# Optimization experiments

Measured on AMD Instinct MI355X. Metric: run time of the kernel, lower is better.

## Reference

```python
import jax, jax.numpy as jnp
import numpy as np

B, S = 8, 2048
DQ = DK = DV = 64


def setup_inputs() -> dict:
    key = jax.random.key(0)
    ks = jax.random.split(key, 9)
    s = 1.0 / np.sqrt(DK)
    return {
        "query": jax.random.normal(ks[0], (B, S, DQ), dtype=jnp.float32),
        "key": jax.random.normal(ks[1], (B, S, DK), dtype=jnp.float32),
        "value": jax.random.normal(ks[2], (B, S, DV), dtype=jnp.float32),
        "inv_scale_factor": jnp.ones((1,), dtype=jnp.float32),
        "dropout_p": jnp.zeros((1,), dtype=jnp.float32),
        "Wq": (jax.random.uniform(ks[3], (DQ, DK), jnp.float32, -1, 1) * s),
        "bq": (jax.random.uniform(ks[4], (DK,), jnp.float32, -1, 1) * s),
        "Wk": (jax.random.uniform(ks[5], (DK, DK), jnp.float32, -1, 1) * s),
        "bk": (jax.random.uniform(ks[6], (DK,), jnp.float32, -1, 1) * s),
        "Wv": (jax.random.uniform(ks[7], (DV, DV), jnp.float32, -1, 1) * s),
        "bv": (jax.random.uniform(ks[8], (DV,), jnp.float32, -1, 1) * s),
    }


def reference(query, key, value, inv_scale_factor, dropout_p, Wq, bq, Wk, bk, Wv, bv):
    # Linear projections (torch Linear: x @ W^T + b; here W stored as [in,out])
    q = query @ Wq + bq              # [B,S,DK]
    k = key @ Wk + bk                # [B,S,DK]
    v = value @ Wv + bv              # [B,S,DV]
    qk = jnp.einsum("bqd,bkd->bqk", q, k)      # [B,S,S]
    scaled_qk = qk / inv_scale_factor[0]
    softmax_qk = jax.nn.softmax(scaled_qk, axis=-1)
    # dropout (training semantics of F.dropout): keep mask / (1-p)
    p = dropout_p[0]
    keep = jax.random.uniform(jax.random.key(42), softmax_qk.shape) >= p
    dropout_qk = jnp.where(keep, softmax_qk, 0.0) / (1.0 - p)
    return jnp.einsum("bqk,bkd->bqd", dropout_qk, v)  # [B,S,DV]
```

## Files before the change

kernel.cpp:

```cpp
#include <hip/hip_runtime.h>
#include <hip/hip_bf16.h>

#define B_ 8
#define S_ 2048
#define D_ 64

using short8  = __attribute__((ext_vector_type(8))) short;
using bf16x4  = __attribute__((ext_vector_type(4))) short;
using f32x4   = __attribute__((ext_vector_type(4))) float;
using uint4v  = __attribute__((ext_vector_type(4))) unsigned int;

typedef unsigned short ushort_t;

static __device__ inline unsigned short f2bf(float f) {
  __hip_bfloat16 h = __float2bfloat16(f);
  return *reinterpret_cast<unsigned short*>(&h);
}
static __device__ inline unsigned int packbf(float a, float b) {
  return (unsigned int)f2bf(a) | ((unsigned int)f2bf(b) << 16);
}

__global__ __launch_bounds__(256) void proj_all(
    const float* __restrict__ query, const float* __restrict__ key,
    const float* __restrict__ value, const float* __restrict__ inv_scale,
    const float* __restrict__ Wq, const float* __restrict__ bq,
    const float* __restrict__ Wk, const float* __restrict__ bk,
    const float* __restrict__ Wv, const float* __restrict__ bv,
    ushort_t* __restrict__ qp, ushort_t* __restrict__ kp,
    ushort_t* __restrict__ vt) {
  __shared__ ushort_t wt[64 * 80];

  int t     = blockIdx.x >> 8;
  int r_    = blockIdx.x & 255;
  int chunk = (r_ & 7) * 32 + (r_ >> 3);
  const float* X    = (t == 0) ? query : (t == 1) ? key : value;
  const float* W    = (t == 0) ? Wq    : (t == 1) ? Wk  : Wv;
  const float* bias = (t == 0) ? bq    : (t == 1) ? bk  : bv;
  float qscale = (t == 0) ? (1.44269504f / inv_scale[0]) : 1.0f;

  {
    int k  = threadIdx.x >> 2;
    int c0 = (threadIdx.x & 3) * 16;
    const float* wr = W + k * 64 + c0;
    #pragma unroll
    for (int j = 0; j < 16; j += 4) {
      float4 v4 = *reinterpret_cast<const float4*>(wr + j);
      wt[(c0 + j)     * 80 + k] = f2bf(v4.x);
      wt[(c0 + j + 1) * 80 + k] = f2bf(v4.y);
      wt[(c0 + j + 2) * 80 + k] = f2bf(v4.z);
      wt[(c0 + j + 3) * 80 + k] = f2bf(v4.w);
    }
  }
  __syncthreads();

  int wv = threadIdx.x >> 6, l = threadIdx.x & 63;
  int lm = l & 15, lh = l >> 4;
  int r0 = chunk * 64 + wv * 16;

  const float* xrow = X + (size_t)(r0 + lm) * 64 + lh * 8;
  float4 x0 = *reinterpret_cast<const float4*>(xrow);
  float4 x1 = *reinterpret_cast<const float4*>(xrow + 4);
  float4 x2 = *reinterpret_cast<const float4*>(xrow + 32);
  float4 x3 = *reinterpret_cast<const float4*>(xrow + 36);
  short8 xa0, xa1;
  xa0[0] = f2bf(x0.x); xa0[1] = f2bf(x0.y); xa0[2] = f2bf(x0.z); xa0[3] = f2bf(x0.w);
  xa0[4] = f2bf(x1.x); xa0[5] = f2bf(x1.y); xa0[6] = f2bf(x1.z); xa0[7] = f2bf(x1.w);
  xa1[0] = f2bf(x2.x); xa1[1] = f2bf(x2.y); xa1[2] = f2bf(x2.z); xa1[3] = f2bf(x2.w);
  xa1[4] = f2bf(x3.x); xa1[5] = f2bf(x3.y); xa1[6] = f2bf(x3.z); xa1[7] = f2bf(x3.w);

  f32x4 zero = {0.f, 0.f, 0.f, 0.f};

  #pragma unroll
  for (int c = 0; c < 4; ++c) {
    const ushort_t* wb = &wt[(c * 16 + lm) * 80 + lh * 8];
    short8 wf0 = *reinterpret_cast<const short8*>(wb);
    short8 wf1 = *reinterpret_cast<const short8*>(wb + 32);

    if (t < 2) {
      f32x4 acc = __builtin_amdgcn_mfma_f32_16x16x32_bf16(wf0, xa0, zero, 0, 0, 0);
      acc       = __builtin_amdgcn_mfma_f32_16x16x32_bf16(wf1, xa1, acc,  0, 0, 0);
      float4 bb = *reinterpret_cast<const float4*>(bias + c * 16 + 4 * lh);
      bf16x4 s;
      s[0] = f2bf((acc[0] + bb.x) * qscale);
      s[1] = f2bf((acc[1] + bb.y) * qscale);
      s[2] = f2bf((acc[2] + bb.z) * qscale);
      s[3] = f2bf((acc[3] + bb.w) * qscale);
      ushort_t* dst = (t ? kp : qp) + (size_t)(r0 + lm) * 64 + c * 16 + 4 * lh;
      *reinterpret_cast<bf16x4*>(dst) = s;
    } else {
      f32x4 acc = __builtin_amdgcn_mfma_f32_16x16x32_bf16(xa0, wf0, zero, 0, 0, 0);
      acc       = __builtin_amdgcn_mfma_f32_16x16x32_bf16(xa1, wf1, acc,  0, 0, 0);
      float bb = bias[c * 16 + lm];
      bf16x4 s;
      s[0] = f2bf(acc[0] + bb); s[1] = f2bf(acc[1] + bb);
      s[2] = f2bf(acc[2] + bb); s[3] = f2bf(acc[3] + bb);
      int bb_i = r0 >> 11;
      int rb   = r0 & 2047;
      int blk  = rb >> 5;
      int th   = (rb >> 4) & 1;
      ushort_t* dst = vt + (((size_t)(bb_i * (S_ / 32) + blk) * 64
                             + c * 16 + lm) * 32) + lh * 8 + 4 * th;
      *reinterpret_cast<bf16x4*>(dst) = s;
    }
  }
}

#define ITERS2 16

__global__ __launch_bounds__(512, 2) void attn(
    const ushort_t* __restrict__ qp, const ushort_t* __restrict__ kp,
    const ushort_t* __restrict__ vt,
    const float* __restrict__ dropout_p, float* __restrict__ out) {
  __shared__ ushort_t kst[4][2][2048];
  __shared__ ushort_t vst[4][2][2048];
  __shared__ float obuf[8][64][33];
  __shared__ float lbuf[8][32];

  const int tid = threadIdx.x;
  const int w = tid >> 6, l = tid & 63;
  const int lm = l & 15, lh = l >> 4;
  const int qi = w & 1, kvs = w >> 1;
  const int b  = blockIdx.x & 7;
  const int qg = blockIdx.x >> 3;
  const int qb = qg * 64 + qi * 32;

  float dscale = 1.0f / (1.0f - dropout_p[0]);

  const ushort_t* qbase = qp + ((size_t)(b * S_ + qb + lm)) * D_ + lh * 8;
  short8 qa0 = *reinterpret_cast<const short8*>(qbase);
  short8 qa1 = *reinterpret_cast<const short8*>(qbase + 32);
  short8 qb0 = *reinterpret_cast<const short8*>(qbase + 16 * D_);
  short8 qb1 = *reinterpret_cast<const short8*>(qbase + 16 * D_ + 32);

  const ushort_t* ksrc = kp + (size_t)b * S_ * D_ + (size_t)kvs * 512 * D_;
  const ushort_t* vsrc = vt + (size_t)(b * 64 + kvs * 16) * 2048;
  const ushort_t* src  = qi ? vsrc : ksrc;

  int swoff[4];
  #pragma unroll
  for (int j = 0; j < 4; ++j) {
    int lin = j * 1024 + l * 16;
    int sw  = qi ? (((l >> 2) & 3) << 4) : (((l >> 3) & 7) << 4);
    swoff[j] = lin ^ sw;
  }
  char* dst0 = qi ? (char*)&vst[kvs][0][0] : (char*)&kst[kvs][0][0];

  const char* kstb = (const char*)&kst[kvs][0][0];
  const char* vstb = (const char*)&vst[kvs][0][0];
  const int kro0 = (lm * 128 + lh * 16)        ^ ((lm & 7) << 4);
  const int kro1 = (lm * 128 + 64 + lh * 16)   ^ ((lm & 7) << 4);
  const int kro2 = ((16 + lm) * 128 + lh * 16) ^ ((lm & 7) << 4);
  const int kro3 = ((16 + lm) * 128 + 64 + lh * 16) ^ ((lm & 7) << 4);
  int vro[4];
  #pragma unroll
  for (int dt = 0; dt < 4; ++dt)
    vro[dt] = ((dt * 16 + lm) * 64 + lh * 16) ^ ((lm & 3) << 4);

  {
    short8 s0 = *reinterpret_cast<const short8*>(src + l * 8);
    short8 s1 = *reinterpret_cast<const short8*>(src + 512 + l * 8);
    short8 s2 = *reinterpret_cast<const short8*>(src + 1024 + l * 8);
    short8 s3 = *reinterpret_cast<const short8*>(src + 1536 + l * 8);
    *reinterpret_cast<short8*>(dst0 + swoff[0]) = s0;
    *reinterpret_cast<short8*>(dst0 + swoff[1]) = s1;
    *reinterpret_cast<short8*>(dst0 + swoff[2]) = s2;
    *reinterpret_cast<short8*>(dst0 + swoff[3]) = s3;
  }
  __syncthreads();

  f32x4 zero = {0.f, 0.f, 0.f, 0.f};
  f32x4 oA[4] = {zero, zero, zero, zero};
  f32x4 oB[4] = {zero, zero, zero, zero};
  float lA = 0.f, lB = 0.f;

  #pragma unroll
  for (int it = 0; it < ITERS2; ++it) {
    const int par = it & 1;

    short8 sg0, sg1, sg2, sg3;
    if (it < ITERS2 - 1) {
      const ushort_t* s = src + (size_t)(it + 1) * 2048;
      sg0 = *reinterpret_cast<const short8*>(s + l * 8);
      sg1 = *reinterpret_cast<const short8*>(s + 512 + l * 8);
      sg2 = *reinterpret_cast<const short8*>(s + 1024 + l * 8);
      sg3 = *reinterpret_cast<const short8*>(s + 1536 + l * 8);
    }

    const char* kb = kstb + par * 4096;
    const char* vb = vstb + par * 4096;
    short8 kf00 = *reinterpret_cast<const short8*>(kb + kro0);
    short8 kf01 = *reinterpret_cast<const short8*>(kb + kro1);
    short8 kf10 = *reinterpret_cast<const short8*>(kb + kro2);
    short8 kf11 = *reinterpret_cast<const short8*>(kb + kro3);
    short8 vf0  = *reinterpret_cast<const short8*>(vb + vro[0]);
    short8 vf1  = *reinterpret_cast<const short8*>(vb + vro[1]);
    short8 vf2  = *reinterpret_cast<const short8*>(vb + vro[2]);
    short8 vf3  = *reinterpret_cast<const short8*>(vb + vro[3]);

    f32x4 ca0 = __builtin_amdgcn_mfma_f32_16x16x32_bf16(kf00, qa0, zero, 0, 0, 0);
    ca0       = __builtin_amdgcn_mfma_f32_16x16x32_bf16(kf01, qa1, ca0,  0, 0, 0);
    f32x4 ca1 = __builtin_amdgcn_mfma_f32_16x16x32_bf16(kf10, qa0, zero, 0, 0, 0);
    ca1       = __builtin_amdgcn_mfma_f32_16x16x32_bf16(kf11, qa1, ca1,  0, 0, 0);
    f32x4 cb0 = __builtin_amdgcn_mfma_f32_16x16x32_bf16(kf00, qb0, zero, 0, 0, 0);
    cb0       = __builtin_amdgcn_mfma_f32_16x16x32_bf16(kf01, qb1, cb0,  0, 0, 0);
    f32x4 cb1 = __builtin_amdgcn_mfma_f32_16x16x32_bf16(kf10, qb0, zero, 0, 0, 0);
    cb1       = __builtin_amdgcn_mfma_f32_16x16x32_bf16(kf11, qb1, cb1,  0, 0, 0);

    float pA0 = __builtin_amdgcn_exp2f(ca0[0]);
    float pA1 = __builtin_amdgcn_exp2f(ca0[1]);
    float pA2 = __builtin_amdgcn_exp2f(ca0[2]);
    float pA3 = __builtin_amdgcn_exp2f(ca0[3]);
    float pA4 = __builtin_amdgcn_exp2f(ca1[0]);
    float pA5 = __builtin_amdgcn_exp2f(ca1[1]);
    float pA6 = __builtin_amdgcn_exp2f(ca1[2]);
    float pA7 = __builtin_amdgcn_exp2f(ca1[3]);
    float pB0 = __builtin_amdgcn_exp2f(cb0[0]);
    float pB1 = __builtin_amdgcn_exp2f(cb0[1]);
    float pB2 = __builtin_amdgcn_exp2f(cb0[2]);
    float pB3 = __builtin_amdgcn_exp2f(cb0[3]);
    float pB4 = __builtin_amdgcn_exp2f(cb1[0]);
    float pB5 = __builtin_amdgcn_exp2f(cb1[1]);
    float pB6 = __builtin_amdgcn_exp2f(cb1[2]);
    float pB7 = __builtin_amdgcn_exp2f(cb1[3]);

    lA += ((pA0 + pA1) + (pA2 + pA3)) + ((pA4 + pA5) + (pA6 + pA7));
    lB += ((pB0 + pB1) + (pB2 + pB3)) + ((pB4 + pB5) + (pB6 + pB7));

    uint4v wa, wb2;
    wa[0]  = packbf(pA0, pA1); wa[1]  = packbf(pA2, pA3);
    wa[2]  = packbf(pA4, pA5); wa[3]  = packbf(pA6, pA7);
    wb2[0] = packbf(pB0, pB1); wb2[1] = packbf(pB2, pB3);
    wb2[2] = packbf(pB4, pB5); wb2[3] = packbf(pB6, pB7);
    short8 paA = *reinterpret_cast<short8*>(&wa);
    short8 paB = *reinterpret_cast<short8*>(&wb2);

    oA[0] = __builtin_amdgcn_mfma_f32_16x16x32_bf16(vf0, paA, oA[0], 0, 0, 0);
    oB[0] = __builtin_amdgcn_mfma_f32_16x16x32_bf16(vf0, paB, oB[0], 0, 0, 0);
    oA[1] = __builtin_amdgcn_mfma_f32_16x16x32_bf16(vf1, paA, oA[1], 0, 0, 0);
    oB[1] = __builtin_amdgcn_mfma_f32_16x16x32_bf16(vf1, paB, oB[1], 0, 0, 0);
    oA[2] = __builtin_amdgcn_mfma_f32_16x16x32_bf16(vf2, paA, oA[2], 0, 0, 0);
    oB[2] = __builtin_amdgcn_mfma_f32_16x16x32_bf16(vf2, paB, oB[2], 0, 0, 0);
    oA[3] = __builtin_amdgcn_mfma_f32_16x16x32_bf16(vf3, paA, oA[3], 0, 0, 0);
    oB[3] = __builtin_amdgcn_mfma_f32_16x16x32_bf16(vf3, paB, oB[3], 0, 0, 0);

    if (it < ITERS2 - 1) {
      char* d = dst0 + (par ^ 1) * 4096;
      *reinterpret_cast<short8*>(d + swoff[0]) = sg0;
      *reinterpret_cast<short8*>(d + swoff[1]) = sg1;
      *reinterpret_cast<short8*>(d + swoff[2]) = sg2;
      *reinterpret_cast<short8*>(d + swoff[3]) = sg3;
    }
    __syncthreads();
  }

  lA += __shfl_xor(lA, 16); lA += __shfl_xor(lA, 32);
  lB += __shfl_xor(lB, 16); lB += __shfl_xor(lB, 32);

  #pragma unroll
  for (int dt = 0; dt < 4; ++dt)
    #pragma unroll
    for (int r = 0; r < 4; ++r) {
      obuf[w][dt * 16 + 4 * lh + r][lm]      = oA[dt][r];
      obuf[w][dt * 16 + 4 * lh + r][16 + lm] = oB[dt][r];
    }
  if (lh == 0) { lbuf[w][lm] = lA; lbuf[w][16 + lm] = lB; }
  __syncthreads();

  int q    = tid >> 3;
  int qih  = q >> 5;
  int qoff = q & 31;
  int d0   = (tid & 7) * 8;
  float L = 0.f;
  #pragma unroll
  for (int kk = 0; kk < 4; ++kk) L += lbuf[kk * 2 + qih][qoff];
  float sc = dscale / L;

  float acc[8];
  #pragma unroll
  for (int jj = 0; jj < 8; ++jj) {
    float s = 0.f;
    #pragma unroll
    for (int kk = 0; kk < 4; ++kk) s += obuf[kk * 2 + qih][d0 + jj][qoff];
    acc[jj] = s * sc;
  }
  float* dst = out + ((size_t)(b * S_ + qg * 64 + q)) * D_ + d0;
  float4 v0 = {acc[0], acc[1], acc[2], acc[3]};
  float4 v1 = {acc[4], acc[5], acc[6], acc[7]};
  *reinterpret_cast<float4*>(dst)     = v0;
  *reinterpret_cast<float4*>(dst + 4) = v1;
}

extern "C" void kernel_launch(void* const* d_in, const int* in_sizes, int n_in,
                              void* d_out, int out_size, void* d_ws, size_t ws_size,
                              hipStream_t stream) {
  const float* query = (const float*)d_in[0];
  const float* key   = (const float*)d_in[1];
  const float* value = (const float*)d_in[2];
  const float* invs  = (const float*)d_in[3];
  const float* dropp = (const float*)d_in[4];
  const float* Wq    = (const float*)d_in[5];
  const float* bq    = (const float*)d_in[6];
  const float* Wk    = (const float*)d_in[7];
  const float* bk    = (const float*)d_in[8];
  const float* Wv    = (const float*)d_in[9];
  const float* bv    = (const float*)d_in[10];
  float* out = (float*)d_out;

  ushort_t* qp = (ushort_t*)d_ws;
  ushort_t* kp = qp + (size_t)B_ * S_ * D_;
  ushort_t* vt = kp + (size_t)B_ * S_ * D_;

  proj_all<<<3 * 256, 256, 0, stream>>>(query, key, value, invs,
                                        Wq, bq, Wk, bk, Wv, bv, qp, kp, vt);
  attn<<<256, 512, 0, stream>>>(qp, kp, vt, dropp, out);
}
```

Measured before the change: 25.45 us.

## Stage K/V tiles via direct global-to-LDS loads and precompute bf16 weights

The attention kernel now copies K/V tiles straight from global memory into LDS with global_load_lds, instead of loading into registers and storing to LDS after the MFMAs. Both tiles use one unified XOR swizzle, and the main loop is no longer forced to unroll. Weight transpose and bf16 conversion, with the q scale folded into Wq and bq, move to a small separate prep kernel. This drops the per-block LDS weight staging and sync in the projection, but adds a third kernel launch and relies on the swizzled source addressing matching the LDS layout, plus async-load completion ordering at the barrier.

```diff
diff --git a/kernel.cpp b/kernel.cpp
--- a/kernel.cpp
+++ b/kernel.cpp
@@ -20,38 +20,52 @@
   return (unsigned int)f2bf(a) | ((unsigned int)f2bf(b) << 16);
 }
 
-__global__ __launch_bounds__(256) void proj_all(
-    const float* __restrict__ query, const float* __restrict__ key,
-    const float* __restrict__ value, const float* __restrict__ inv_scale,
+static __device__ __forceinline__ void gl16(const void* g, void* l) {
+  __builtin_amdgcn_global_load_lds(
+      (const __attribute__((address_space(1))) void*)g,
+      (__attribute__((address_space(3))) void*)l, 16, 0, 0);
+}
+static __device__ __forceinline__ int swz(int lin) {
+  return lin ^ (((lin >> 7) & 7) << 4);
+}
+
+__global__ __launch_bounds__(256) void prep_w(
     const float* __restrict__ Wq, const float* __restrict__ bq,
     const float* __restrict__ Wk, const float* __restrict__ bk,
     const float* __restrict__ Wv, const float* __restrict__ bv,
+    const float* __restrict__ inv_scale,
+    ushort_t* __restrict__ wt3, float* __restrict__ b3) {
+  int t = blockIdx.x;
+  const float* W    = (t == 0) ? Wq : (t == 1) ? Wk : Wv;
+  const float* bias = (t == 0) ? bq : (t == 1) ? bk : bv;
+  float s = (t == 0) ? (1.44269504f / inv_scale[0]) : 1.0f;
+  int k  = threadIdx.x >> 2;
+  int c0 = (threadIdx.x & 3) * 16;
+  const float* wr = W + k * 64 + c0;
+  ushort_t* dst = wt3 + t * 4096;
+  #pragma unroll
+  for (int j = 0; j < 16; j += 4) {
+    float4 v4 = *reinterpret_cast<const float4*>(wr + j);
+    dst[(c0 + j)     * 64 + k] = f2bf(v4.x * s);
+    dst[(c0 + j + 1) * 64 + k] = f2bf(v4.y * s);
+    dst[(c0 + j + 2) * 64 + k] = f2bf(v4.z * s);
+    dst[(c0 + j + 3) * 64 + k] = f2bf(v4.w * s);
+  }
+  if (threadIdx.x < 64) b3[t * 64 + threadIdx.x] = bias[threadIdx.x] * s;
+}
+
+__global__ __launch_bounds__(256) void proj_all(
+    const float* __restrict__ query, const float* __restrict__ key,
+    const float* __restrict__ value,
+    const ushort_t* __restrict__ wt3, const float* __restrict__ b3,
     ushort_t* __restrict__ qp, ushort_t* __restrict__ kp,
     ushort_t* __restrict__ vt) {
-  __shared__ ushort_t wt[64 * 80];
-
   int t     = blockIdx.x >> 8;
   int r_    = blockIdx.x & 255;
   int chunk = (r_ & 7) * 32 + (r_ >> 3);
-  const float* X    = (t == 0) ? query : (t == 1) ? key : value;
-  const float* W    = (t == 0) ? Wq    : (t == 1) ? Wk  : Wv;
-  const float* bias = (t == 0) ? bq    : (t == 1) ? bk  : bv;
-  float qscale = (t == 0) ? (1.44269504f / inv_scale[0]) : 1.0f;
-
-  {
-    int k  = threadIdx.x >> 2;
-    int c0 = (threadIdx.x & 3) * 16;
-    const float* wr = W + k * 64 + c0;
-    #pragma unroll
-    for (int j = 0; j < 16; j += 4) {
-      float4 v4 = *reinterpret_cast<const float4*>(wr + j);
-      wt[(c0 + j)     * 80 + k] = f2bf(v4.x);
-      wt[(c0 + j + 1) * 80 + k] = f2bf(v4.y);
-      wt[(c0 + j + 2) * 80 + k] = f2bf(v4.z);
-      wt[(c0 + j + 3) * 80 + k] = f2bf(v4.w);
-    }
-  }
-  __syncthreads();
+  const float* X        = (t == 0) ? query : (t == 1) ? key : value;
+  const ushort_t* wtb   = wt3 + t * 4096;
+  const float* bias     = b3 + t * 64;
 
   int wv = threadIdx.x >> 6, l = threadIdx.x & 63;
   int lm = l & 15, lh = l >> 4;
@@ -72,7 +86,7 @@
 
   #pragma unroll
   for (int c = 0; c < 4; ++c) {
-    const ushort_t* wb = &wt[(c * 16 + lm) * 80 + lh * 8];
+    const ushort_t* wb = wtb + (c * 16 + lm) * 64 + lh * 8;
     short8 wf0 = *reinterpret_cast<const short8*>(wb);
     short8 wf1 = *reinterpret_cast<const short8*>(wb + 32);
 
@@ -81,10 +95,8 @@
       acc       = __builtin_amdgcn_mfma_f32_16x16x32_bf16(wf1, xa1, acc,  0, 0, 0);
       float4 bb = *reinterpret_cast<const float4*>(bias + c * 16 + 4 * lh);
       bf16x4 s;
-      s[0] = f2bf((acc[0] + bb.x) * qscale);
-      s[1] = f2bf((acc[1] + bb.y) * qscale);
-      s[2] = f2bf((acc[2] + bb.z) * qscale);
-      s[3] = f2bf((acc[3] + bb.w) * qscale);
+      s[0] = f2bf(acc[0] + bb.x); s[1] = f2bf(acc[1] + bb.y);
+      s[2] = f2bf(acc[2] + bb.z); s[3] = f2bf(acc[3] + bb.w);
       ushort_t* dst = (t ? kp : qp) + (size_t)(r0 + lm) * 64 + c * 16 + 4 * lh;
       *reinterpret_cast<bf16x4*>(dst) = s;
     } else {
@@ -111,8 +123,8 @@
     const ushort_t* __restrict__ qp, const ushort_t* __restrict__ kp,
     const ushort_t* __restrict__ vt,
     const float* __restrict__ dropout_p, float* __restrict__ out) {
-  __shared__ ushort_t kst[4][2][2048];
-  __shared__ ushort_t vst[4][2][2048];
+  __shared__ __align__(16) ushort_t kst[4][2][2048];
+  __shared__ __align__(16) ushort_t vst[4][2][2048];
   __shared__ float obuf[8][64][33];
   __shared__ float lbuf[8][32];
 
@@ -132,40 +144,29 @@
   short8 qb0 = *reinterpret_cast<const short8*>(qbase + 16 * D_);
   short8 qb1 = *reinterpret_cast<const short8*>(qbase + 16 * D_ + 32);
 
-  const ushort_t* ksrc = kp + (size_t)b * S_ * D_ + (size_t)kvs * 512 * D_;
-  const ushort_t* vsrc = vt + (size_t)(b * 64 + kvs * 16) * 2048;
-  const ushort_t* src  = qi ? vsrc : ksrc;
-
-  int swoff[4];
-  #pragma unroll
-  for (int j = 0; j < 4; ++j) {
-    int lin = j * 1024 + l * 16;
-    int sw  = qi ? (((l >> 2) & 3) << 4) : (((l >> 3) & 7) << 4);
-    swoff[j] = lin ^ sw;
-  }
-  char* dst0 = qi ? (char*)&vst[kvs][0][0] : (char*)&kst[kvs][0][0];
+  const char* ksrc = (const char*)kp + ((size_t)(b * S_ + kvs * 512)) * D_ * 2;
+  const char* vsrc = (const char*)vt + ((size_t)(b * 64 + kvs * 16)) * 4096;
+  const char* src0 = qi ? vsrc : ksrc;
+  char* ldsb = qi ? (char*)&vst[kvs][0][0] : (char*)&kst[kvs][0][0];
+
+  int soff[4];
+  #pragma unroll
+  for (int j = 0; j < 4; ++j) soff[j] = swz(j * 1024 + l * 16);
 
   const char* kstb = (const char*)&kst[kvs][0][0];
   const char* vstb = (const char*)&vst[kvs][0][0];
-  const int kro0 = (lm * 128 + lh * 16)        ^ ((lm & 7) << 4);
-  const int kro1 = (lm * 128 + 64 + lh * 16)   ^ ((lm & 7) << 4);
-  const int kro2 = ((16 + lm) * 128 + lh * 16) ^ ((lm & 7) << 4);
-  const int kro3 = ((16 + lm) * 128 + 64 + lh * 16) ^ ((lm & 7) << 4);
+  const int kro0 = swz(lm * 128 + lh * 16);
+  const int kro1 = swz(lm * 128 + 64 + lh * 16);
+  const int kro2 = swz((16 + lm) * 128 + lh * 16);
+  const int kro3 = swz((16 + lm) * 128 + 64 + lh * 16);
   int vro[4];
   #pragma unroll
   for (int dt = 0; dt < 4; ++dt)
-    vro[dt] = ((dt * 16 + lm) * 64 + lh * 16) ^ ((lm & 3) << 4);
-
-  {
-    short8 s0 = *reinterpret_cast<const short8*>(src + l * 8);
-    short8 s1 = *reinterpret_cast<const short8*>(src + 512 + l * 8);
-    short8 s2 = *reinterpret_cast<const short8*>(src + 1024 + l * 8);
-    short8 s3 = *reinterpret_cast<const short8*>(src + 1536 + l * 8);
-    *reinterpret_cast<short8*>(dst0 + swoff[0]) = s0;
-    *reinterpret_cast<short8*>(dst0 + swoff[1]) = s1;
-    *reinterpret_cast<short8*>(dst0 + swoff[2]) = s2;
-    *reinterpret_cast<short8*>(dst0 + swoff[3]) = s3;
-  }
+    vro[dt] = swz((dt * 16 + lm) * 64 + lh * 16);
+
+  #pragma unroll
+  for (int j = 0; j < 4; ++j)
+    gl16(src0 + soff[j], ldsb + j * 1024);
   __syncthreads();
 
   f32x4 zero = {0.f, 0.f, 0.f, 0.f};
@@ -173,17 +174,15 @@
   f32x4 oB[4] = {zero, zero, zero, zero};
   float lA = 0.f, lB = 0.f;
 
-  #pragma unroll
   for (int it = 0; it < ITERS2; ++it) {
     const int par = it & 1;
 
-    short8 sg0, sg1, sg2, sg3;
     if (it < ITERS2 - 1) {
-      const ushort_t* s = src + (size_t)(it + 1) * 2048;
-      sg0 = *reinterpret_cast<const short8*>(s + l * 8);
-      sg1 = *reinterpret_cast<const short8*>(s + 512 + l * 8);
-      sg2 = *reinterpret_cast<const short8*>(s + 1024 + l * 8);
-      sg3 = *reinterpret_cast<const short8*>(s + 1536 + l * 8);
+      const char* s = src0 + (size_t)(it + 1) * 4096;
+      char* d = ldsb + (par ^ 1) * 4096;
+      #pragma unroll
+      for (int j = 0; j < 4; ++j)
+        gl16(s + soff[j], d + j * 1024);
     }
 
     const char* kb = kstb + par * 4096;
@@ -243,13 +242,6 @@
     oA[3] = __builtin_amdgcn_mfma_f32_16x16x32_bf16(vf3, paA, oA[3], 0, 0, 0);
     oB[3] = __builtin_amdgcn_mfma_f32_16x16x32_bf16(vf3, paB, oB[3], 0, 0, 0);
 
-    if (it < ITERS2 - 1) {
-      char* d = dst0 + (par ^ 1) * 4096;
-      *reinterpret_cast<short8*>(d + swoff[0]) = sg0;
-      *reinterpret_cast<short8*>(d + swoff[1]) = sg1;
-      *reinterpret_cast<short8*>(d + swoff[2]) = sg2;
-      *reinterpret_cast<short8*>(d + swoff[3]) = sg3;
-    }
     __syncthreads();
   }
 
@@ -306,11 +298,13 @@
   const float* bv    = (const float*)d_in[10];
   float* out = (float*)d_out;
 
-  ushort_t* qp = (ushort_t*)d_ws;
-  ushort_t* kp = qp + (size_t)B_ * S_ * D_;
-  ushort_t* vt = kp + (size_t)B_ * S_ * D_;
-
-  proj_all<<<3 * 256, 256, 0, stream>>>(query, key, value, invs,
-                                        Wq, bq, Wk, bk, Wv, bv, qp, kp, vt);
+  ushort_t* qp  = (ushort_t*)d_ws;
+  ushort_t* kp  = qp + (size_t)B_ * S_ * D_;
+  ushort_t* vt  = kp + (size_t)B_ * S_ * D_;
+  ushort_t* wt3 = vt + (size_t)B_ * S_ * D_;
+  float*    b3  = (float*)(wt3 + 3 * 4096);
+
+  prep_w<<<3, 256, 0, stream>>>(Wq, bq, Wk, bk, Wv, bv, invs, wt3, b3);
+  proj_all<<<3 * 256, 256, 0, stream>>>(query, key, value, wt3, b3, qp, kp, vt);
   attn<<<256, 512, 0, stream>>>(qp, kp, vt, dropp, out);
 }
```

After: 31.78 us. 1.25x slower.

## Load V fragments directly from global into registers, stage only K in LDS

Applied to the files above, without the earlier changes.

V tiles are no longer staged through shared memory. Each wave now loads its own V MFMA fragments straight from the pre-transposed global layout into registers and prefetches the next tile one iteration ahead. K loading is split across both q-waves, each loading half, with a uniform XOR swizzle, and the main loop is no longer fully unrolled. This halves LDS footprint and LDS traffic, but each wave pair now loads V redundantly from global/L2, register pressure rises, and dropping the unroll may add loop overhead.

```diff
diff --git a/kernel.cpp b/kernel.cpp
--- a/kernel.cpp
+++ b/kernel.cpp
@@ -18,6 +18,9 @@
 }
 static __device__ inline unsigned int packbf(float a, float b) {
   return (unsigned int)f2bf(a) | ((unsigned int)f2bf(b) << 16);
+}
+static __device__ __forceinline__ int swz(int lin) {
+  return lin ^ (((lin >> 7) & 7) << 4);
 }
 
 __global__ __launch_bounds__(256) void proj_all(
@@ -111,8 +114,7 @@
     const ushort_t* __restrict__ qp, const ushort_t* __restrict__ kp,
     const ushort_t* __restrict__ vt,
     const float* __restrict__ dropout_p, float* __restrict__ out) {
-  __shared__ ushort_t kst[4][2][2048];
-  __shared__ ushort_t vst[4][2][2048];
+  __shared__ __align__(16) ushort_t kst[4][2][2048];
   __shared__ float obuf[8][64][33];
   __shared__ float lbuf[8][32];
 
@@ -132,40 +134,31 @@
   short8 qb0 = *reinterpret_cast<const short8*>(qbase + 16 * D_);
   short8 qb1 = *reinterpret_cast<const short8*>(qbase + 16 * D_ + 32);
 
-  const ushort_t* ksrc = kp + (size_t)b * S_ * D_ + (size_t)kvs * 512 * D_;
-  const ushort_t* vsrc = vt + (size_t)(b * 64 + kvs * 16) * 2048;
-  const ushort_t* src  = qi ? vsrc : ksrc;
-
-  int swoff[4];
-  #pragma unroll
-  for (int j = 0; j < 4; ++j) {
-    int lin = j * 1024 + l * 16;
-    int sw  = qi ? (((l >> 2) & 3) << 4) : (((l >> 3) & 7) << 4);
-    swoff[j] = lin ^ sw;
-  }
-  char* dst0 = qi ? (char*)&vst[kvs][0][0] : (char*)&kst[kvs][0][0];
-
-  const char* kstb = (const char*)&kst[kvs][0][0];
-  const char* vstb = (const char*)&vst[kvs][0][0];
-  const int kro0 = (lm * 128 + lh * 16)        ^ ((lm & 7) << 4);
-  const int kro1 = (lm * 128 + 64 + lh * 16)   ^ ((lm & 7) << 4);
-  const int kro2 = ((16 + lm) * 128 + lh * 16) ^ ((lm & 7) << 4);
-  const int kro3 = ((16 + lm) * 128 + 64 + lh * 16) ^ ((lm & 7) << 4);
-  int vro[4];
-  #pragma unroll
-  for (int dt = 0; dt < 4; ++dt)
-    vro[dt] = ((dt * 16 + lm) * 64 + lh * 16) ^ ((lm & 3) << 4);
+  const char* ksg = (const char*)kp + ((size_t)(b * S_ + kvs * 512)) * D_ * 2;
+  const int gofs0 = qi * 2048 + l * 16;
+  const int gofs1 = qi * 2048 + 1024 + l * 16;
+  const int swo0  = swz(gofs0);
+  const int swo1  = swz(gofs1);
+  char* kstb = (char*)&kst[kvs][0][0];
+
+  const int kro0 = swz(lm * 128 + lh * 16);
+  const int kro1 = swz(lm * 128 + 64 + lh * 16);
+  const int kro2 = swz((16 + lm) * 128 + lh * 16);
+  const int kro3 = swz((16 + lm) * 128 + 64 + lh * 16);
+
+  const ushort_t* vbl = vt + ((size_t)(b * 64 + kvs * 16)) * 2048
+                           + lm * 32 + lh * 8;
 
   {
-    short8 s0 = *reinterpret_cast<const short8*>(src + l * 8);
-    short8 s1 = *reinterpret_cast<const short8*>(src + 512 + l * 8);
-    short8 s2 = *reinterpret_cast<const short8*>(src + 1024 + l * 8);
-    short8 s3 = *reinterpret_cast<const short8*>(src + 1536 + l * 8);
-    *reinterpret_cast<short8*>(dst0 + swoff[0]) = s0;
-    *reinterpret_cast<short8*>(dst0 + swoff[1]) = s1;
-    *reinterpret_cast<short8*>(dst0 + swoff[2]) = s2;
-    *reinterpret_cast<short8*>(dst0 + swoff[3]) = s3;
-  }
+    short8 k0 = *reinterpret_cast<const short8*>(ksg + gofs0);
+    short8 k1 = *reinterpret_cast<const short8*>(ksg + gofs1);
+    *reinterpret_cast<short8*>(kstb + swo0) = k0;
+    *reinterpret_cast<short8*>(kstb + swo1) = k1;
+  }
+  short8 vc0 = *reinterpret_cast<const short8*>(vbl);
+  short8 vc1 = *reinterpret_cast<const short8*>(vbl + 512);
+  short8 vc2 = *reinterpret_cast<const short8*>(vbl + 1024);
+  short8 vc3 = *reinterpret_cast<const short8*>(vbl + 1536);
   __syncthreads();
 
   f32x4 zero = {0.f, 0.f, 0.f, 0.f};
@@ -173,29 +166,23 @@
   f32x4 oB[4] = {zero, zero, zero, zero};
   float lA = 0.f, lB = 0.f;
 
-  #pragma unroll
   for (int it = 0; it < ITERS2; ++it) {
     const int par = it & 1;
-
-    short8 sg0, sg1, sg2, sg3;
-    if (it < ITERS2 - 1) {
-      const ushort_t* s = src + (size_t)(it + 1) * 2048;
-      sg0 = *reinterpret_cast<const short8*>(s + l * 8);
-      sg1 = *reinterpret_cast<const short8*>(s + 512 + l * 8);
-      sg2 = *reinterpret_cast<const short8*>(s + 1024 + l * 8);
-      sg3 = *reinterpret_cast<const short8*>(s + 1536 + l * 8);
-    }
+    const int nit = (it + 1 < ITERS2) ? it + 1 : it;
+
+    short8 kr0 = *reinterpret_cast<const short8*>(ksg + (size_t)nit * 4096 + gofs0);
+    short8 kr1 = *reinterpret_cast<const short8*>(ksg + (size_t)nit * 4096 + gofs1);
+    const ushort_t* vn = vbl + (size_t)nit * 2048;
+    short8 vn0 = *reinterpret_cast<const short8*>(vn);
+    short8 vn1 = *reinterpret_cast<const short8*>(vn + 512);
+    short8 vn2 = *reinterpret_cast<const short8*>(vn + 1024);
+    short8 vn3 = *reinterpret_cast<const short8*>(vn + 1536);
 
     const char* kb = kstb + par * 4096;
-    const char* vb = vstb + par * 4096;
     short8 kf00 = *reinterpret_cast<const short8*>(kb + kro0);
     short8 kf01 = *reinterpret_cast<const short8*>(kb + kro1);
     short8 kf10 = *reinterpret_cast<const short8*>(kb + kro2);
     short8 kf11 = *reinterpret_cast<const short8*>(kb + kro3);
-    short8 vf0  = *reinterpret_cast<const short8*>(vb + vro[0]);
-    short8 vf1  = *reinterpret_cast<const short8*>(vb + vro[1]);
-    short8 vf2  = *reinterpret_cast<const short8*>(vb + vro[2]);
-    short8 vf3  = *reinterpret_cast<const short8*>(vb + vro[3]);
 
     f32x4 ca0 = __builtin_amdgcn_mfma_f32_16x16x32_bf16(kf00, qa0, zero, 0, 0, 0);
     ca0       = __builtin_amdgcn_mfma_f32_16x16x32_bf16(kf01, qa1, ca0,  0, 0, 0);
@@ -234,23 +221,23 @@
     short8 paA = *reinterpret_cast<short8*>(&wa);
     short8 paB = *reinterpret_cast<short8*>(&wb2);
 
-    oA[0] = __builtin_amdgcn_mfma_f32_16x16x32_bf16(vf0, paA, oA[0], 0, 0, 0);
-    oB[0] = __builtin_amdgcn_mfma_f32_16x16x32_bf16(vf0, paB, oB[0], 0, 0, 0);
-    oA[1] = __builtin_amdgcn_mfma_f32_16x16x32_bf16(vf1, paA, oA[1], 0, 0, 0);
-    oB[1] = __builtin_amdgcn_mfma_f32_16x16x32_bf16(vf1, paB, oB[1], 0, 0, 0);
-    oA[2] = __builtin_amdgcn_mfma_f32_16x16x32_bf16(vf2, paA, oA[2], 0, 0, 0);
-    oB[2] = __builtin_amdgcn_mfma_f32_16x16x32_bf16(vf2, paB, oB[2], 0, 0, 0);
-    oA[3] = __builtin_amdgcn_mfma_f32_16x16x32_bf16(vf3, paA, oA[3], 0, 0, 0);
-    oB[3] = __builtin_amdgcn_mfma_f32_16x16x32_bf16(vf3, paB, oB[3], 0, 0, 0);
+    oA[0] = __builtin_amdgcn_mfma_f32_16x16x32_bf16(vc0, paA, oA[0], 0, 0, 0);
+    oB[0] = __builtin_amdgcn_mfma_f32_16x16x32_bf16(vc0, paB, oB[0], 0, 0, 0);
+    oA[1] = __builtin_amdgcn_mfma_f32_16x16x32_bf16(vc1, paA, oA[1], 0, 0, 0);
+    oB[1] = __builtin_amdgcn_mfma_f32_16x16x32_bf16(vc1, paB, oB[1], 0, 0, 0);
+    oA[2] = __builtin_amdgcn_mfma_f32_16x16x32_bf16(vc2, paA, oA[2], 0, 0, 0);
+    oB[2] = __builtin_amdgcn_mfma_f32_16x16x32_bf16(vc2, paB, oB[2], 0, 0, 0);
+    oA[3] = __builtin_amdgcn_mfma_f32_16x16x32_bf16(vc3, paA, oA[3], 0, 0, 0);
+    oB[3] = __builtin_amdgcn_mfma_f32_16x16x32_bf16(vc3, paB, oB[3], 0, 0, 0);
 
     if (it < ITERS2 - 1) {
-      char* d = dst0 + (par ^ 1) * 4096;
-      *reinterpret_cast<short8*>(d + swoff[0]) = sg0;
-      *reinterpret_cast<short8*>(d + swoff[1]) = sg1;
-      *reinterpret_cast<short8*>(d + swoff[2]) = sg2;
-      *reinterpret_cast<short8*>(d + swoff[3]) = sg3;
+      char* d = kstb + (par ^ 1) * 4096;
+      *reinterpret_cast<short8*>(d + swo0) = kr0;
+      *reinterpret_cast<short8*>(d + swo1) = kr1;
     }
     __syncthreads();
+
+    vc0 = vn0; vc1 = vn1; vc2 = vn2; vc3 = vn3;
   }
 
   lA += __shfl_xor(lA, 16); lA += __shfl_xor(lA, 32);
```

Result: slower. 27.27 us (+7.2%).
